# Kernel tuning notes

Measured on AMD Instinct MI355X. Metric: run time of the kernel, lower is better.

## Reference

```python
import jax, jax.numpy as jnp
import numpy as np

N_NODES = 50000
N_EDGES = 600000
IN_DIM = 128
HIDDEN = 128


def setup_inputs() -> dict:
    key = jax.random.key(0)
    k1, k2, k3, k4 = jax.random.split(key, 4)
    x = jax.random.normal(k1, (N_NODES, IN_DIM), dtype=jnp.float32)
    edge_index = jax.random.randint(k2, (2, N_EDGES), 0, N_NODES, dtype=jnp.int64)
    # Glorot-ish init for the two GCN layer weights
    W1 = jax.random.normal(k3, (IN_DIM, HIDDEN), dtype=jnp.float32) / np.sqrt(IN_DIM)
    b1 = jnp.zeros((HIDDEN,), dtype=jnp.float32)
    W2 = jax.random.normal(k4, (HIDDEN, HIDDEN), dtype=jnp.float32) / np.sqrt(HIDDEN)
    b2 = jnp.zeros((HIDDEN,), dtype=jnp.float32)
    return {"x": x, "edge_index": edge_index, "W1": W1, "b1": b1, "W2": W2, "b2": b2}


def _gcn_layer(x, W, b, src, dst, deg_inv_sqrt, n_nodes):
    # GCNConv: out = D^{-1/2} (A + I) D^{-1/2} X W + b, computed edge-wise.
    xw = x @ W                                           # [N, H] dense GEMM
    norm = deg_inv_sqrt[src] * deg_inv_sqrt[dst]         # [E+N]
    msg = xw[src] * norm[:, None]                        # gather + scale, [E+N, H]
    agg = jax.ops.segment_sum(msg, dst, num_segments=n_nodes)  # scatter-add
    return agg + b


def reference(x, edge_index, W1, b1, W2, b2):
    n_nodes = x.shape[0]
    loop = jnp.arange(n_nodes, dtype=edge_index.dtype)
    # add self-loops once; shared by both layers (same graph)
    src = jnp.concatenate([edge_index[0], loop])
    dst = jnp.concatenate([edge_index[1], loop])
    deg = jax.ops.segment_sum(jnp.ones_like(src, dtype=x.dtype), dst, num_segments=n_nodes)
    deg_inv_sqrt = jnp.where(deg > 0, jax.lax.rsqrt(jnp.maximum(deg, 1.0)), 0.0)

    h = jax.nn.relu(_gcn_layer(x, W1, b1, src, dst, deg_inv_sqrt, n_nodes))
    h = jax.nn.relu(_gcn_layer(h, W2, b2, src, dst, deg_inv_sqrt, n_nodes))
    return h
```

## Files before the change

kernel.cpp:

```cpp
#include <hip/hip_runtime.h>
#include <hip/hip_bf16.h>

#define DIM 128
#define CHUNK 4096
#define CAP 4096
typedef __hip_bfloat16 bf16;
typedef __attribute__((ext_vector_type(8))) short bf16x8;
typedef __attribute__((ext_vector_type(4))) float f32x4;

__global__ void prep_kernel(int* __restrict__ bcursor, int nbuck,
                            const int* __restrict__ ei, int E, int* __restrict__ misc,
                            const float* __restrict__ W1, const float* __restrict__ W2,
                            bf16* __restrict__ Wsw1, bf16* __restrict__ Wsw2) {
    if (blockIdx.x == 0) {
        for (int i = threadIdx.x; i < nbuck; i += 256) bcursor[i] = i * CAP;
    } else if (blockIdx.x == 1) {
        __shared__ int s_or;
        if (threadIdx.x == 0) s_or = 0;
        __syncthreads();
        int lim = E < 16384 ? E : 16384;
        int acc = 0;
        for (int j = threadIdx.x; j < lim; j += 256) acc |= ei[2 * j + 1];
        if (acc) atomicOr(&s_or, 1);
        __syncthreads();
        if (threadIdx.x == 0) misc[1] = s_or;
    } else {
        int id = (blockIdx.x - 2) * 256 + threadIdx.x;
        const float* W = (id < 2048) ? W1 : W2;
        bf16* Wsw = (id < 2048) ? Wsw1 : Wsw2;
        int t = id & 2047;
        int f = t >> 6, l = t & 63;
        int kt = f >> 3, nt = f & 7;
        int q = l >> 4, m = l & 15;
        bf16 tmp[8];
        #pragma unroll
        for (int j = 0; j < 8; ++j)
            tmp[j] = __float2bfloat16(W[(size_t)(kt * 32 + q * 8 + j) * DIM + nt * 16 + m]);
        *(bf16x8*)(Wsw + (size_t)t * 8) = *(const bf16x8*)tmp;
    }
}

template <bool XF32>
__device__ __forceinline__ void gemm_body(const void* __restrict__ Xv,
                                          const bf16* __restrict__ Wsw,
                                          bf16* __restrict__ Y, int N,
                                          int gw, int nw, int lane,
                                          float* sld) {
    int m = lane & 15, q = lane >> 4;
    const bf16x8* bp = (const bf16x8*)Wsw;
    for (int t = gw; t * 16 + 16 <= N; t += nw) {
        int base = t * 16;
        bf16x8 a[4];
        if (XF32) {
            const float* xp = (const float*)Xv + (size_t)(base + m) * DIM + q * 8;
            #pragma unroll
            for (int kt = 0; kt < 4; ++kt) {
                float4 v0 = *(const float4*)(xp + kt * 32);
                float4 v1 = *(const float4*)(xp + kt * 32 + 4);
                bf16 tt[8] = {__float2bfloat16(v0.x), __float2bfloat16(v0.y),
                              __float2bfloat16(v0.z), __float2bfloat16(v0.w),
                              __float2bfloat16(v1.x), __float2bfloat16(v1.y),
                              __float2bfloat16(v1.z), __float2bfloat16(v1.w)};
                a[kt] = *(const bf16x8*)tt;
            }
        } else {
            const bf16* xp = (const bf16*)Xv + (size_t)(base + m) * DIM + q * 8;
            #pragma unroll
            for (int kt = 0; kt < 4; ++kt)
                a[kt] = *(const bf16x8*)(xp + kt * 32);
        }
        f32x4 acc[8];
        #pragma unroll
        for (int nt = 0; nt < 8; ++nt) acc[nt] = (f32x4){0.f, 0.f, 0.f, 0.f};
        #pragma unroll
        for (int kt = 0; kt < 4; ++kt) {
            #pragma unroll
            for (int nt = 0; nt < 8; ++nt) {
                bf16x8 bfr = bp[(size_t)(kt * 8 + nt) * 64 + lane];
                acc[nt] = __builtin_amdgcn_mfma_f32_16x16x32_bf16(a[kt], bfr, acc[nt], 0, 0, 0);
            }
        }
        #pragma unroll
        for (int nt = 0; nt < 8; ++nt)
            #pragma unroll
            for (int r = 0; r < 4; ++r)
                sld[(q * 4 + r) * 132 + nt * 16 + m] = acc[nt][r];
        asm volatile("s_waitcnt lgkmcnt(0)" ::: "memory");
        #pragma unroll
        for (int i = 0; i < 4; ++i) {
            int row = i * 4 + q;
            const float* rp = sld + row * 132 + m * 8;
            float4 v0 = *(const float4*)rp;
            float4 v1 = *(const float4*)(rp + 4);
            alignas(16) bf16 tt[8] = {
                __float2bfloat16(v0.x), __float2bfloat16(v0.y),
                __float2bfloat16(v0.z), __float2bfloat16(v0.w),
                __float2bfloat16(v1.x), __float2bfloat16(v1.y),
                __float2bfloat16(v1.z), __float2bfloat16(v1.w)};
            *(uint4*)(Y + (size_t)(base + row) * DIM + m * 8) = *(const uint4*)tt;
        }
        asm volatile("s_waitcnt lgkmcnt(0)" ::: "memory");
    }
}

__global__ __launch_bounds__(256)
void scatter_gemm1(const int* __restrict__ ei, int E, const int* __restrict__ misc,
                   int* __restrict__ bcursor, unsigned* __restrict__ staged,
                   int nbuck, int nchunks,
                   const float* __restrict__ X, const bf16* __restrict__ Wsw,
                   bf16* __restrict__ Y, int N) {
    __shared__ float smem[4][16 * 132];
    int bx = blockIdx.x;
    if (bx < nchunks) {
        int* s_cnt  = (int*)&smem[0][0];
        int* s_base = s_cnt + 512;
        int* s_fill = s_cnt + 1024;
        for (int i = threadIdx.x; i < nbuck; i += 256) { s_cnt[i] = 0; s_fill[i] = 0; }
        __syncthreads();
        int flagI = misc[1];
        int c0 = bx * CHUNK;
        int cn = min(E - c0, CHUNK);
        for (int i = threadIdx.x; i < cn; i += 256) {
            int e = c0 + i;
            int d = (flagI == 0) ? ei[2 * E + 2 * e] : ei[E + e];
            atomicAdd(&s_cnt[d >> 7], 1);
        }
        __syncthreads();
        for (int i = threadIdx.x; i < nbuck; i += 256) {
            int c = s_cnt[i];
            s_base[i] = c ? atomicAdd(&bcursor[i], c) : 0;
        }
        __syncthreads();
        for (int i = threadIdx.x; i < cn; i += 256) {
            int e = c0 + i;
            int s, d;
            if (flagI == 0) { s = ei[2 * e]; d = ei[2 * E + 2 * e]; }
            else            { s = ei[e];     d = ei[E + e]; }
            int b = d >> 7;
            int r = s_base[b] + atomicAdd(&s_fill[b], 1);
            if (r < (b + 1) * CAP)
                staged[r] = ((unsigned)s << 7) | (unsigned)(d & 127);
        }
    } else {
        int wid = threadIdx.x >> 6, lane = threadIdx.x & 63;
        int ngw = (gridDim.x - nchunks) * 4;
        gemm_body<true>(X, Wsw, Y, N, (bx - nchunks) * 4 + wid, ngw, lane, smem[wid]);
    }
}

__global__ void bucket_sort(const unsigned* __restrict__ staged,
                            const int* __restrict__ bcursor,
                            int* __restrict__ csr, int* __restrict__ rowstart,
                            int* __restrict__ cnt, float* __restrict__ dis, int N) {
    __shared__ int s_cnt[128], s_off[128], s_fill[128], s_scan[128];
    int b = blockIdx.x, tid = threadIdx.x;
    int seg0 = b * CAP;
    int n = min(bcursor[b] - seg0, CAP);
    if (tid < 128) { s_cnt[tid] = 0; s_fill[tid] = 0; }
    __syncthreads();
    for (int i = tid; i < n; i += 256)
        atomicAdd(&s_cnt[staged[seg0 + i] & 127u], 1);
    __syncthreads();
    int v = (tid < 128) ? s_cnt[tid] : 0;
    if (tid < 128) s_scan[tid] = v;
    __syncthreads();
    for (int off = 1; off < 128; off <<= 1) {
        int t = (tid < 128 && tid >= off) ? s_scan[tid - off] : 0;
        __syncthreads();
        if (tid < 128) s_scan[tid] += t;
        __syncthreads();
    }
    if (tid < 128) {
        s_off[tid] = s_scan[tid] - v;
        int node = b * 128 + tid;
        if (node < N) {
            cnt[node] = v;
            rowstart[node] = seg0 + s_off[tid];
            dis[node] = rsqrtf((float)(v + 1));
        }
    }
    __syncthreads();
    for (int i = tid; i < n; i += 256) {
        unsigned p = staged[seg0 + i];
        int dl = p & 127u;
        int r = atomicAdd(&s_fill[dl], 1);
        csr[seg0 + s_off[dl] + r] = (int)(p >> 7);
    }
}

__global__ __launch_bounds__(256)
void gemm2(const bf16* __restrict__ H, const bf16* __restrict__ Wsw,
           bf16* __restrict__ Y, int N) {
    __shared__ float smem[4][16 * 132];
    int wid = threadIdx.x >> 6, lane = threadIdx.x & 63;
    gemm_body<false>(H, Wsw, Y, N, blockIdx.x * 4 + wid, gridDim.x * 4, lane, smem[wid]);
}

__device__ __forceinline__ void fma8(float* a, uint4 v, float ds) {
    a[0] = fmaf(__uint_as_float(v.x << 16), ds, a[0]);
    a[1] = fmaf(__uint_as_float(v.x & 0xffff0000u), ds, a[1]);
    a[2] = fmaf(__uint_as_float(v.y << 16), ds, a[2]);
    a[3] = fmaf(__uint_as_float(v.y & 0xffff0000u), ds, a[3]);
    a[4] = fmaf(__uint_as_float(v.z << 16), ds, a[4]);
    a[5] = fmaf(__uint_as_float(v.z & 0xffff0000u), ds, a[5]);
    a[6] = fmaf(__uint_as_float(v.w << 16), ds, a[6]);
    a[7] = fmaf(__uint_as_float(v.w & 0xffff0000u), ds, a[7]);
}

template <bool FINAL>
__global__ __launch_bounds__(256, 4)
void aggregate_bf(const uint4* __restrict__ Y, const int* __restrict__ rowstart,
                  const int* __restrict__ cnt, const int* __restrict__ csr,
                  const float* __restrict__ dis, const float* __restrict__ bias,
                  uint4* __restrict__ Hb, float4* __restrict__ Of, int N) {
    int wave = threadIdx.x >> 6;
    int lane = threadIdx.x & 63;
    int sub = lane >> 4, cl = lane & 15;
    int node = blockIdx.x * 16 + wave * 4 + sub;
    if (node >= N) return;
    int e0 = rowstart[node], e1 = e0 + cnt[node];

    float acc[4][8];
    #pragma unroll
    for (int j = 0; j < 4; ++j)
        #pragma unroll
        for (int k = 0; k < 8; ++k) acc[j][k] = 0.f;

    float dn = dis[node];
    fma8(acc[3], Y[(size_t)node * 16 + cl], dn);

    int e = e0;
    while (e + 8 <= e1) {
        int s[8];
        #pragma unroll
        for (int j = 0; j < 8; ++j) s[j] = csr[e + j];
        uint4 v[8]; float dv[8];
        #pragma unroll
        for (int j = 0; j < 8; ++j) { v[j] = Y[(size_t)s[j] * 16 + cl]; dv[j] = dis[s[j]]; }
        #pragma unroll
        for (int j = 0; j < 8; ++j) fma8(acc[j & 3], v[j], dv[j]);
        e += 8;
    }
    if (e + 4 <= e1) {
        int s[4];
        #pragma unroll
        for (int j = 0; j < 4; ++j) s[j] = csr[e + j];
        uint4 v[4]; float dv[4];
        #pragma unroll
        for (int j = 0; j < 4; ++j) { v[j] = Y[(size_t)s[j] * 16 + cl]; dv[j] = dis[s[j]]; }
        #pragma unroll
        for (int j = 0; j < 4; ++j) fma8(acc[j], v[j], dv[j]);
        e += 4;
    }
    for (; e < e1; ++e) {
        int s = csr[e];
        fma8(acc[0], Y[(size_t)s * 16 + cl], dis[s]);
    }

    float s8[8];
    #pragma unroll
    for (int k = 0; k < 8; ++k)
        s8[k] = (acc[0][k] + acc[1][k]) + (acc[2][k] + acc[3][k]);

    float4 b0 = ((const float4*)bias)[2 * cl];
    float4 b1 = ((const float4*)bias)[2 * cl + 1];
    float o[8];
    o[0] = fmaxf(dn * s8[0] + b0.x, 0.f);
    o[1] = fmaxf(dn * s8[1] + b0.y, 0.f);
    o[2] = fmaxf(dn * s8[2] + b0.z, 0.f);
    o[3] = fmaxf(dn * s8[3] + b0.w, 0.f);
    o[4] = fmaxf(dn * s8[4] + b1.x, 0.f);
    o[5] = fmaxf(dn * s8[5] + b1.y, 0.f);
    o[6] = fmaxf(dn * s8[6] + b1.z, 0.f);
    o[7] = fmaxf(dn * s8[7] + b1.w, 0.f);
    if (FINAL) {
        Of[(size_t)node * 32 + 2 * cl]     = make_float4(o[0], o[1], o[2], o[3]);
        Of[(size_t)node * 32 + 2 * cl + 1] = make_float4(o[4], o[5], o[6], o[7]);
    } else {
        bf16 t[8];
        #pragma unroll
        for (int k = 0; k < 8; ++k) t[k] = __float2bfloat16(o[k]);
        Hb[(size_t)node * 16 + cl] = *(const uint4*)t;
    }
}

extern "C" void kernel_launch(void* const* d_in, const int* in_sizes, int n_in,
                              void* d_out, int out_size, void* d_ws, size_t ws_size,
                              hipStream_t stream) {
    const float* x  = (const float*)d_in[0];
    const int*   ei = (const int*)d_in[1];
    const float* W1 = (const float*)d_in[2];
    const float* b1 = (const float*)d_in[3];
    const float* W2 = (const float*)d_in[4];
    const float* b2 = (const float*)d_in[5];

    int N = in_sizes[0] / DIM;
    int E = in_sizes[1] / 2;
    int nbuck = (N + 127) / 128;
    int nchunks = (E + CHUNK - 1) / CHUNK;

    char* w = (char*)d_ws;
    size_t used = 0;
    auto carve = [&](size_t bytes) {
        char* p = w + used;
        used += (bytes + 255) & ~(size_t)255;
        return p;
    };
    int*      misc     = (int*)     carve(256);
    int*      bcursor  = (int*)     carve((size_t)(nbuck + 1) * 4);
    unsigned* staged   = (unsigned*)carve((size_t)nbuck * CAP * 4);
    int*      csr      = (int*)     carve((size_t)nbuck * CAP * 4);
    int*      rowstart = (int*)     carve((size_t)N * 4);
    int*      cnt      = (int*)     carve((size_t)N * 4);
    float*    dis      = (float*)   carve((size_t)N * 4);
    bf16*     ybuf     = (bf16*)    carve((size_t)N * DIM * 2);
    bf16*     hbuf     = (bf16*)    carve((size_t)N * DIM * 2);
    bf16*     Wsw1     = (bf16*)    carve((size_t)DIM * DIM * 2);
    bf16*     Wsw2     = (bf16*)    carve((size_t)DIM * DIM * 2);

    prep_kernel <<<18, 256, 0, stream>>>(bcursor, nbuck, ei, E, misc, W1, W2, Wsw1, Wsw2);
    scatter_gemm1<<<nchunks + 784, 256, 0, stream>>>(ei, E, misc, bcursor, staged,
                                                     nbuck, nchunks, x, Wsw1, ybuf, N);
    bucket_sort <<<nbuck, 256, 0, stream>>>(staged, bcursor, csr, rowstart, cnt, dis, N);

    int ablocks = (N + 15) / 16;
    aggregate_bf<false><<<ablocks, 256, 0, stream>>>((const uint4*)ybuf, rowstart, cnt,
                                                     csr, dis, b1, (uint4*)hbuf, nullptr, N);
    gemm2<<<784, 256, 0, stream>>>(hbuf, Wsw2, ybuf, N);
    aggregate_bf<true><<<ablocks, 256, 0, stream>>>((const uint4*)ybuf, rowstart, cnt,
                                                    csr, dis, b2, nullptr, (float4*)d_out, N);
}
```

Measured before the change: 190.8 us.

## Fuse layer-1 aggregation with second GEMM and prescale source rows

```diff
diff --git a/kernel.cpp b/kernel.cpp
--- a/kernel.cpp
+++ b/kernel.cpp
@@ -188,14 +188,6 @@
     }
 }
 
-__global__ __launch_bounds__(256)
-void gemm2(const bf16* __restrict__ H, const bf16* __restrict__ Wsw,
-           bf16* __restrict__ Y, int N) {
-    __shared__ float smem[4][16 * 132];
-    int wid = threadIdx.x >> 6, lane = threadIdx.x & 63;
-    gemm_body<false>(H, Wsw, Y, N, blockIdx.x * 4 + wid, gridDim.x * 4, lane, smem[wid]);
-}
-
 __device__ __forceinline__ void fma8(float* a, uint4 v, float ds) {
     a[0] = fmaf(__uint_as_float(v.x << 16), ds, a[0]);
     a[1] = fmaf(__uint_as_float(v.x & 0xffff0000u), ds, a[1]);
@@ -207,12 +199,136 @@
     a[7] = fmaf(__uint_as_float(v.w & 0xffff0000u), ds, a[7]);
 }
 
-template <bool FINAL>
+__device__ __forceinline__ void add8(float* a, uint4 v) {
+    a[0] += __uint_as_float(v.x << 16);
+    a[1] += __uint_as_float(v.x & 0xffff0000u);
+    a[2] += __uint_as_float(v.y << 16);
+    a[3] += __uint_as_float(v.y & 0xffff0000u);
+    a[4] += __uint_as_float(v.z << 16);
+    a[5] += __uint_as_float(v.z & 0xffff0000u);
+    a[6] += __uint_as_float(v.w << 16);
+    a[7] += __uint_as_float(v.w & 0xffff0000u);
+}
+
 __global__ __launch_bounds__(256, 4)
-void aggregate_bf(const uint4* __restrict__ Y, const int* __restrict__ rowstart,
-                  const int* __restrict__ cnt, const int* __restrict__ csr,
-                  const float* __restrict__ dis, const float* __restrict__ bias,
-                  uint4* __restrict__ Hb, float4* __restrict__ Of, int N) {
+void agg1_gemm2(const uint4* __restrict__ Y, const int* __restrict__ rowstart,
+                const int* __restrict__ cnt, const int* __restrict__ csr,
+                const float* __restrict__ dis, const float* __restrict__ bias,
+                const bf16* __restrict__ Wsw, bf16* __restrict__ Y2, int N) {
+    __shared__ __align__(16) bf16 h_lds[16][136];
+    __shared__ float s_out[16 * 132];
+    int wave = threadIdx.x >> 6, lane = threadIdx.x & 63;
+    int sub = lane >> 4, cl = lane & 15;
+    int base = blockIdx.x * 16;
+    int node = base + wave * 4 + sub;
+    bool alive = node < N;
+
+    float acc[4][8];
+    #pragma unroll
+    for (int j = 0; j < 4; ++j)
+        #pragma unroll
+        for (int k = 0; k < 8; ++k) acc[j][k] = 0.f;
+
+    float dn = 0.f;
+    if (alive) {
+        int e0 = rowstart[node], e1 = e0 + cnt[node];
+        dn = dis[node];
+        fma8(acc[3], Y[(size_t)node * 16 + cl], dn);
+
+        int e = e0;
+        while (e + 8 <= e1) {
+            int s[8];
+            #pragma unroll
+            for (int j = 0; j < 8; ++j) s[j] = csr[e + j];
+            uint4 v[8]; float dv[8];
+            #pragma unroll
+            for (int j = 0; j < 8; ++j) { v[j] = Y[(size_t)s[j] * 16 + cl]; dv[j] = dis[s[j]]; }
+            #pragma unroll
+            for (int j = 0; j < 8; ++j) fma8(acc[j & 3], v[j], dv[j]);
+            e += 8;
+        }
+        if (e + 4 <= e1) {
+            int s[4];
+            #pragma unroll
+            for (int j = 0; j < 4; ++j) s[j] = csr[e + j];
+            uint4 v[4]; float dv[4];
+            #pragma unroll
+            for (int j = 0; j < 4; ++j) { v[j] = Y[(size_t)s[j] * 16 + cl]; dv[j] = dis[s[j]]; }
+            #pragma unroll
+            for (int j = 0; j < 4; ++j) fma8(acc[j], v[j], dv[j]);
+            e += 4;
+        }
+        for (; e < e1; ++e) {
+            int s = csr[e];
+            fma8(acc[0], Y[(size_t)s * 16 + cl], dis[s]);
+        }
+    }
+    {
+        float s8[8];
+        #pragma unroll
+        for (int k = 0; k < 8; ++k)
+            s8[k] = (acc[0][k] + acc[1][k]) + (acc[2][k] + acc[3][k]);
+        float4 b0 = ((const float4*)bias)[2 * cl];
+        float4 b1 = ((const float4*)bias)[2 * cl + 1];
+        alignas(16) bf16 t[8];
+        t[0] = __float2bfloat16(alive ? fmaxf(dn * s8[0] + b0.x, 0.f) : 0.f);
+        t[1] = __float2bfloat16(alive ? fmaxf(dn * s8[1] + b0.y, 0.f) : 0.f);
+        t[2] = __float2bfloat16(alive ? fmaxf(dn * s8[2] + b0.z, 0.f) : 0.f);
+        t[3] = __float2bfloat16(alive ? fmaxf(dn * s8[3] + b0.w, 0.f) : 0.f);
+        t[4] = __float2bfloat16(alive ? fmaxf(dn * s8[4] + b1.x, 0.f) : 0.f);
+        t[5] = __float2bfloat16(alive ? fmaxf(dn * s8[5] + b1.y, 0.f) : 0.f);
+        t[6] = __float2bfloat16(alive ? fmaxf(dn * s8[6] + b1.z, 0.f) : 0.f);
+        t[7] = __float2bfloat16(alive ? fmaxf(dn * s8[7] + b1.w, 0.f) : 0.f);
+        *(uint4*)&h_lds[wave * 4 + sub][cl * 8] = *(const uint4*)t;
+    }
+    __syncthreads();
+
+    int m = cl, q = sub;
+    bf16x8 a[4];
+    #pragma unroll
+    for (int kt = 0; kt < 4; ++kt)
+        a[kt] = *(const bf16x8*)&h_lds[m][q * 8 + kt * 32];
+    const bf16x8* bp = (const bf16x8*)Wsw;
+    f32x4 g[2];
+    g[0] = (f32x4){0.f, 0.f, 0.f, 0.f};
+    g[1] = (f32x4){0.f, 0.f, 0.f, 0.f};
+    #pragma unroll
+    for (int kt = 0; kt < 4; ++kt) {
+        #pragma unroll
+        for (int j = 0; j < 2; ++j) {
+            int nt = wave * 2 + j;
+            bf16x8 bfr = bp[(size_t)(kt * 8 + nt) * 64 + lane];
+            g[j] = __builtin_amdgcn_mfma_f32_16x16x32_bf16(a[kt], bfr, g[j], 0, 0, 0);
+        }
+    }
+    #pragma unroll
+    for (int j = 0; j < 2; ++j)
+        #pragma unroll
+        for (int r = 0; r < 4; ++r)
+            s_out[(q * 4 + r) * 132 + (wave * 2 + j) * 16 + m] = g[j][r];
+    __syncthreads();
+
+    int on = threadIdx.x >> 4;
+    int oc = (threadIdx.x & 15) * 8;
+    if (base + on < N) {
+        float ds = dis[base + on];
+        const float* rp = s_out + on * 132 + oc;
+        float4 v0 = *(const float4*)rp;
+        float4 v1 = *(const float4*)(rp + 4);
+        alignas(16) bf16 t[8] = {
+            __float2bfloat16(v0.x * ds), __float2bfloat16(v0.y * ds),
+            __float2bfloat16(v0.z * ds), __float2bfloat16(v0.w * ds),
+            __float2bfloat16(v1.x * ds), __float2bfloat16(v1.y * ds),
+            __float2bfloat16(v1.z * ds), __float2bfloat16(v1.w * ds)};
+        *(uint4*)(Y2 + (size_t)(base + on) * DIM + oc) = *(const uint4*)t;
+    }
+}
+
+__global__ __launch_bounds__(256, 4)
+void aggregate_final(const uint4* __restrict__ Y, const int* __restrict__ rowstart,
+                     const int* __restrict__ cnt, const int* __restrict__ csr,
+                     const float* __restrict__ dis, const float* __restrict__ bias,
+                     float4* __restrict__ Of, int N) {
     int wave = threadIdx.x >> 6;
     int lane = threadIdx.x & 63;
     int sub = lane >> 4, cl = lane & 15;
@@ -227,35 +343,33 @@
         for (int k = 0; k < 8; ++k) acc[j][k] = 0.f;
 
     float dn = dis[node];
-    fma8(acc[3], Y[(size_t)node * 16 + cl], dn);
+    add8(acc[3], Y[(size_t)node * 16 + cl]);
 
     int e = e0;
     while (e + 8 <= e1) {
         int s[8];
         #pragma unroll
         for (int j = 0; j < 8; ++j) s[j] = csr[e + j];
-        uint4 v[8]; float dv[8];
-        #pragma unroll
-        for (int j = 0; j < 8; ++j) { v[j] = Y[(size_t)s[j] * 16 + cl]; dv[j] = dis[s[j]]; }
-        #pragma unroll
-        for (int j = 0; j < 8; ++j) fma8(acc[j & 3], v[j], dv[j]);
+        uint4 v[8];
+        #pragma unroll
+        for (int j = 0; j < 8; ++j) v[j] = Y[(size_t)s[j] * 16 + cl];
+        #pragma unroll
+        for (int j = 0; j < 8; ++j) add8(acc[j & 3], v[j]);
         e += 8;
     }
     if (e + 4 <= e1) {
         int s[4];
         #pragma unroll
         for (int j = 0; j < 4; ++j) s[j] = csr[e + j];
-        uint4 v[4]; float dv[4];
-        #pragma unroll
-        for (int j = 0; j < 4; ++j) { v[j] = Y[(size_t)s[j] * 16 + cl]; dv[j] = dis[s[j]]; }
-        #pragma unroll
-        for (int j = 0; j < 4; ++j) fma8(acc[j], v[j], dv[j]);
+        uint4 v[4];
+        #pragma unroll
+        for (int j = 0; j < 4; ++j) v[j] = Y[(size_t)s[j] * 16 + cl];
+        #pragma unroll
+        for (int j = 0; j < 4; ++j) add8(acc[j], v[j]);
         e += 4;
     }
-    for (; e < e1; ++e) {
-        int s = csr[e];
-        fma8(acc[0], Y[(size_t)s * 16 + cl], dis[s]);
-    }
+    for (; e < e1; ++e)
+        add8(acc[0], Y[(size_t)csr[e] * 16 + cl]);
 
     float s8[8];
     #pragma unroll
@@ -273,15 +387,8 @@
     o[5] = fmaxf(dn * s8[5] + b1.y, 0.f);
     o[6] = fmaxf(dn * s8[6] + b1.z, 0.f);
     o[7] = fmaxf(dn * s8[7] + b1.w, 0.f);
-    if (FINAL) {
-        Of[(size_t)node * 32 + 2 * cl]     = make_float4(o[0], o[1], o[2], o[3]);
-        Of[(size_t)node * 32 + 2 * cl + 1] = make_float4(o[4], o[5], o[6], o[7]);
-    } else {
-        bf16 t[8];
-        #pragma unroll
-        for (int k = 0; k < 8; ++k) t[k] = __float2bfloat16(o[k]);
-        Hb[(size_t)node * 16 + cl] = *(const uint4*)t;
-    }
+    Of[(size_t)node * 32 + 2 * cl]     = make_float4(o[0], o[1], o[2], o[3]);
+    Of[(size_t)node * 32 + 2 * cl + 1] = make_float4(o[4], o[5], o[6], o[7]);
 }
 
 extern "C" void kernel_launch(void* const* d_in, const int* in_sizes, int n_in,
@@ -324,9 +431,8 @@
     bucket_sort <<<nbuck, 256, 0, stream>>>(staged, bcursor, csr, rowstart, cnt, dis, N);
 
     int ablocks = (N + 15) / 16;
-    aggregate_bf<false><<<ablocks, 256, 0, stream>>>((const uint4*)ybuf, rowstart, cnt,
-                                                     csr, dis, b1, (uint4*)hbuf, nullptr, N);
-    gemm2<<<784, 256, 0, stream>>>(hbuf, Wsw2, ybuf, N);
-    aggregate_bf<true><<<ablocks, 256, 0, stream>>>((const uint4*)ybuf, rowstart, cnt,
-                                                    csr, dis, b2, nullptr, (float4*)d_out, N);
-}
+    agg1_gemm2<<<ablocks, 256, 0, stream>>>((const uint4*)ybuf, rowstart, cnt, csr,
+                                            dis, b1, Wsw2, hbuf, N);
+    aggregate_final<<<ablocks, 256, 0, stream>>>((const uint4*)hbuf, rowstart, cnt, csr,
+                                                 dis, b2, (float4*)d_out, N);
+}
```

Result: faster. 181.8 us (-4.7%).
